# Kernel optimization log

Hardware: AMD Instinct MI355X
Metric: run time of the kernel (lower is better)

Reference implementation:

```python
import jax, jax.numpy as jnp
import numpy as np

FS = 2048
LOWER_FREQ = 16.0
UPPER_FREQ = 512.0
N_SCALES = 64
SIZE_FACTOR = 1.0


def _build_ricker_bank():
    # Geometric scale grid from 1/upper_freq to 1/lower_freq
    s0 = 1.0 / UPPER_FREQ
    sn = 1.0 / LOWER_FREQ
    base = np.power(sn / s0, 1.0 / (N_SCALES - 1))
    scales = s0 * np.power(base, np.arange(N_SCALES))  # [n_scales]
    truncation = scales.max() * np.sqrt(4.5) * FS
    one_side = int(SIZE_FACTOR * truncation)
    kernel_size = 2 * one_side + 1  # 543 for these settings
    k = np.arange(kernel_size, dtype=np.float32) - one_side
    t = k / FS  # [K]
    s = scales[:, None].astype(np.float32)  # [n_scales, 1]
    A = 2.0 / (np.sqrt(3.0 * s) * np.pi ** 0.25)
    scaled_t = t[None, :] / s
    bank = A * (1.0 - scaled_t ** 2) * np.exp(-t[None, :] ** 2 / (2.0 * s ** 2))
    return jnp.asarray(bank, dtype=jnp.float32)  # [n_scales, K]


def setup_inputs() -> dict:
    key = jax.random.key(0)
    inputs = jax.random.normal(key, (128, 4096), dtype=jnp.float32)
    W = _build_ricker_bank()  # [64, 543]
    return {"inputs": inputs, "W": W}


def reference(inputs, W):
    # inputs: [B, T]; W: [n_scales, K] Ricker wavelet bank (real-only).
    # Torch does conv2d on [B,1,T,1] with weight [n_scales,1,K,1], padding K//2
    # (K odd -> 'same' length). border_crop=0, imaginary_part=None, so the
    # scalogram is just the real convolution output.
    K = W.shape[1]
    out = jax.lax.conv_general_dilated(
        inputs[:, None, :],          # [B, 1, T]
        W[:, None, :],               # [n_scales, 1, K]
        window_strides=(1,),
        padding=[(K // 2, K // 2)],
        dimension_numbers=("NCH", "OIH", "NCH"),
    )
    return out  # [B, n_scales, T]
```

## Files before the change

kernel.cpp:

```cpp
#include <hip/hip_runtime.h>


#define TLEN  4096
#define NSC   64
#define KLEN  543
#define KPAD  544
#define PADL  271
#define BLOCK 256
#define TT    512
#define XSRC  1056
#define XLEN  1048
#define XREG  1048
#define NKS   34

typedef __attribute__((ext_vector_type(8)))  short  short8;
typedef __attribute__((ext_vector_type(16))) float  float16v;
typedef __attribute__((ext_vector_type(4)))  float  float4v;

__device__ __forceinline__ ushort f2bf(float f) {
    unsigned u = __builtin_bit_cast(unsigned, f);
    unsigned r = (u + 0x7FFFu + ((u >> 16) & 1u)) >> 16;
    return (ushort)r;
}

__global__ __launch_bounds__(256)
void wconv(const float* __restrict__ W, ushort* __restrict__ wpk)
{
    int idx  = blockIdx.x * 256 + threadIdx.x;
    int e    = idx & 7;
    int lane = (idx >> 3) & 63;
    int st   = (idx >> 9) & 1;
    int ks   = idx >> 10;
    int n    = lane & 31;
    int q5   = lane >> 5;
    int s    = 32 * st + n;
    int k    = 16 * ks + 8 * q5 + e;
    float v  = (k < KLEN) ? W[(size_t)s * KLEN + k] : 0.0f;
    wpk[idx] = f2bf(v);
}

__global__ __launch_bounds__(BLOCK, 3)
void ricker_mfma2(const float* __restrict__ x,
                  const ushort* __restrict__ wpk,
                  float* __restrict__ out)
{
    __shared__ __align__(16) ushort xraw[XSRC];
    __shared__ __align__(16) ushort xsm[8 * XREG];

    const int tid    = threadIdx.x;
    const int tTile  = blockIdx.x;
    const int b      = blockIdx.y;
    const int tStart = tTile * TT;

    const float* xrow = x + (size_t)b * TLEN;
    for (int i = tid; i < XSRC; i += BLOCK) {
        int g = tStart - PADL + i;
        float v = (g >= 0 && g < TLEN) ? xrow[g] : 0.0f;
        xraw[i] = f2bf(v);
    }
    __syncthreads();

    {
        const short8* xr8 = (const short8*)xraw;
        short8*       xs8 = (short8*)xsm;
        for (int j = tid; j < 131; j += BLOCK) {
            short8 lo = xr8[j];
            short8 hi = xr8[j + 1];
            #pragma unroll
            for (int c = 0; c < 8; ++c) {
                short8 r;
                #pragma unroll
                for (int e = 0; e < 8; ++e)
                    r[e] = (c + e < 8) ? lo[c + e] : hi[c + e - 8];
                xs8[c * 131 + j] = r;
            }
        }
    }
    __syncthreads();

    const int lane = tid & 63;
    const int wv   = tid >> 6;
    const int n    = lane & 31;
    const int q5   = lane >> 5;
    const int wt0  = wv * 128;

    const ushort* abase = &xsm[(n & 7) * XREG + 8 * (n >> 3) + 8 * q5 + wt0];
    const ushort* bbase = wpk + (size_t)lane * 8;

    float16v acc[4][2];
    #pragma unroll
    for (int tt = 0; tt < 4; ++tt)
        #pragma unroll
        for (int st = 0; st < 2; ++st)
            #pragma unroll
            for (int e = 0; e < 16; ++e) acc[tt][st][e] = 0.f;

    #pragma unroll 2
    for (int ks = 0; ks < NKS; ++ks) {
        const int K0 = 16 * ks;
        const int BO = 1024 * ks;
        short8 bb0 = *(const short8*)&bbase[BO];
        short8 bb1 = *(const short8*)&bbase[BO + 512];
        short8 a[4];
        #pragma unroll
        for (int tt = 0; tt < 4; ++tt)
            a[tt] = *(const short8*)&abase[K0 + 32 * tt];
        __builtin_amdgcn_s_setprio(1);
        #pragma unroll
        for (int tt = 0; tt < 4; ++tt) {
            acc[tt][0] = __builtin_amdgcn_mfma_f32_32x32x16_bf16(a[tt], bb0, acc[tt][0], 0, 0, 0);
            acc[tt][1] = __builtin_amdgcn_mfma_f32_32x32x16_bf16(a[tt], bb1, acc[tt][1], 0, 0, 0);
        }
        __builtin_amdgcn_s_setprio(0);
    }

    const int tb = tStart + wt0 + 4 * q5;
    float* obase = out + (size_t)b * NSC * TLEN;
    #pragma unroll
    for (int st = 0; st < 2; ++st) {
        #pragma unroll
        for (int tt = 0; tt < 4; ++tt) {
            float16v A = acc[tt][st];
            float* o = obase + (size_t)(32 * st + n) * TLEN + tb + 32 * tt;
            #pragma unroll
            for (int r4 = 0; r4 < 4; ++r4) {
                *(float4v*)&o[8 * r4] =
                    (float4v){A[4 * r4], A[4 * r4 + 1], A[4 * r4 + 2], A[4 * r4 + 3]};
            }
        }
    }
}

extern "C" void kernel_launch(void* const* d_in, const int* in_sizes, int n_in,
                              void* d_out, int out_size, void* d_ws, size_t ws_size,
                              hipStream_t stream) {
    const float* x   = (const float*)d_in[0];
    const float* W   = (const float*)d_in[1];
    float*       out = (float*)d_out;
    ushort*      wpk = (ushort*)d_ws;

    wconv<<<dim3((NSC * KPAD) / 256), dim3(256), 0, stream>>>(W, wpk);
    dim3 grid(TLEN / TT, 128);
    ricker_mfma2<<<grid, dim3(BLOCK), 0, stream>>>(x, wpk, out);
}
```

Baseline: 171.1 us.

## Exploit Ricker filter symmetry to halve MFMA work, switch to fp16

Because the Ricker wavelet is symmetric around its center tap, the kernel now adds mirrored input pairs (x[t+d] + x[t-d]) before multiplying, so only half the filter taps (17 K-steps instead of 34) go through MFMA, with the center tap weight halved. The intent is to cut matrix-core work roughly in half at the cost of extra LDS reads and vector fp16 adds. Data and weights switch from bf16 to fp16 for better precision in the pre-added sums, and the occupancy hint drops from 3 to 2 blocks per SM. Precision changes with fp16 range, though the inputs are normal-distributed and well within range.

```diff
diff --git a/kernel.cpp b/kernel.cpp
--- a/kernel.cpp
+++ b/kernel.cpp
@@ -4,27 +4,22 @@
 #define TLEN  4096
 #define NSC   64
 #define KLEN  543
-#define KPAD  544
 #define PADL  271
 #define BLOCK 256
 #define TT    512
 #define XSRC  1056
 #define XLEN  1048
 #define XREG  1048
-#define NKS   34
+#define NKS2  17
+#define WPK_N (NKS2 * 2 * 64 * 8)
 
-typedef __attribute__((ext_vector_type(8)))  short  short8;
-typedef __attribute__((ext_vector_type(16))) float  float16v;
-typedef __attribute__((ext_vector_type(4)))  float  float4v;
-
-__device__ __forceinline__ ushort f2bf(float f) {
-    unsigned u = __builtin_bit_cast(unsigned, f);
-    unsigned r = (u + 0x7FFFu + ((u >> 16) & 1u)) >> 16;
-    return (ushort)r;
-}
+typedef __attribute__((ext_vector_type(8)))  short     short8;
+typedef __attribute__((ext_vector_type(8)))  _Float16  half8;
+typedef __attribute__((ext_vector_type(16))) float     float16v;
+typedef __attribute__((ext_vector_type(4)))  float     float4v;
 
 __global__ __launch_bounds__(256)
-void wconv(const float* __restrict__ W, ushort* __restrict__ wpk)
+void wconv(const float* __restrict__ W, _Float16* __restrict__ wpk)
 {
     int idx  = blockIdx.x * 256 + threadIdx.x;
     int e    = idx & 7;
@@ -34,18 +29,19 @@
     int n    = lane & 31;
     int q5   = lane >> 5;
     int s    = 32 * st + n;
-    int k    = 16 * ks + 8 * q5 + e;
-    float v  = (k < KLEN) ? W[(size_t)s * KLEN + k] : 0.0f;
-    wpk[idx] = f2bf(v);
+    int d    = 16 * ks + 8 * q5 + e;
+    float v  = W[(size_t)s * KLEN + PADL + d];
+    if (d == 0) v *= 0.5f;
+    wpk[idx] = (_Float16)v;
 }
 
-__global__ __launch_bounds__(BLOCK, 3)
+__global__ __launch_bounds__(BLOCK, 2)
 void ricker_mfma2(const float* __restrict__ x,
-                  const ushort* __restrict__ wpk,
+                  const _Float16* __restrict__ wpk,
                   float* __restrict__ out)
 {
-    __shared__ __align__(16) ushort xraw[XSRC];
-    __shared__ __align__(16) ushort xsm[8 * XREG];
+    __shared__ __align__(16) _Float16 xraw[XSRC];
+    __shared__ __align__(16) _Float16 xsm[8 * XREG];
 
     const int tid    = threadIdx.x;
     const int tTile  = blockIdx.x;
@@ -56,7 +52,7 @@
     for (int i = tid; i < XSRC; i += BLOCK) {
         int g = tStart - PADL + i;
         float v = (g >= 0 && g < TLEN) ? xrow[g] : 0.0f;
-        xraw[i] = f2bf(v);
+        xraw[i] = (_Float16)v;
     }
     __syncthreads();
 
@@ -84,8 +80,11 @@
     const int q5   = lane >> 5;
     const int wt0  = wv * 128;
 
-    const ushort* abase = &xsm[(n & 7) * XREG + 8 * (n >> 3) + 8 * q5 + wt0];
-    const ushort* bbase = wpk + (size_t)lane * 8;
+    const int cf = (n + 7) & 7;
+    const int cr = n & 7;
+    const _Float16* af = &xsm[cf * XREG + wt0 + 8 * q5 + (n + PADL - cf)];
+    const _Float16* ar = &xsm[cr * XREG + wt0 - 8 * q5 + 264 + (n - cr)];
+    const _Float16* bbase = wpk + (size_t)lane * 8;
 
     float16v acc[4][2];
     #pragma unroll
@@ -96,22 +95,24 @@
             for (int e = 0; e < 16; ++e) acc[tt][st][e] = 0.f;
 
     #pragma unroll 2
-    for (int ks = 0; ks < NKS; ++ks) {
-        const int K0 = 16 * ks;
+    for (int ks = 0; ks < NKS2; ++ks) {
+        const int KF = 16 * ks;
         const int BO = 1024 * ks;
-        short8 bb0 = *(const short8*)&bbase[BO];
-        short8 bb1 = *(const short8*)&bbase[BO + 512];
-        short8 a[4];
-        #pragma unroll
-        for (int tt = 0; tt < 4; ++tt)
-            a[tt] = *(const short8*)&abase[K0 + 32 * tt];
-        __builtin_amdgcn_s_setprio(1);
+        half8 bb0 = *(const half8*)&bbase[BO];
+        half8 bb1 = *(const half8*)&bbase[BO + 512];
+        half8 z[4];
         #pragma unroll
         for (int tt = 0; tt < 4; ++tt) {
-            acc[tt][0] = __builtin_amdgcn_mfma_f32_32x32x16_bf16(a[tt], bb0, acc[tt][0], 0, 0, 0);
-            acc[tt][1] = __builtin_amdgcn_mfma_f32_32x32x16_bf16(a[tt], bb1, acc[tt][1], 0, 0, 0);
+            half8 f = *(const half8*)&af[KF + 32 * tt];
+            half8 r = *(const half8*)&ar[32 * tt - KF];
+            half8 rv = __builtin_shufflevector(r, r, 7, 6, 5, 4, 3, 2, 1, 0);
+            z[tt] = f + rv;
         }
-        __builtin_amdgcn_s_setprio(0);
+        #pragma unroll
+        for (int tt = 0; tt < 4; ++tt) {
+            acc[tt][0] = __builtin_amdgcn_mfma_f32_32x32x16_f16(z[tt], bb0, acc[tt][0], 0, 0, 0);
+            acc[tt][1] = __builtin_amdgcn_mfma_f32_32x32x16_f16(z[tt], bb1, acc[tt][1], 0, 0, 0);
+        }
     }
 
     const int tb = tStart + wt0 + 4 * q5;
@@ -137,9 +138,9 @@
     const float* x   = (const float*)d_in[0];
     const float* W   = (const float*)d_in[1];
     float*       out = (float*)d_out;
-    ushort*      wpk = (ushort*)d_ws;
+    _Float16*    wpk = (_Float16*)d_ws;
 
-    wconv<<<dim3((NSC * KPAD) / 256), dim3(256), 0, stream>>>(W, wpk);
+    wconv<<<dim3(WPK_N / 256), dim3(256), 0, stream>>>(W, wpk);
     dim3 grid(TLEN / TT, 128);
     ricker_mfma2<<<grid, dim3(BLOCK), 0, stream>>>(x, wpk, out);
 }
```

Measured after the change: 153.4 us. -10.3%, faster.
